# Optimization experiments

Measured on AMD Instinct MI355X. Metric: run time of the kernel, lower is better.

Reference implementation:

```python
import jax, jax.numpy as jnp
import numpy as np

SPACING = 0.25
CHANNELS = 32
MAX_VAL = 5.0
ENC_FEATS = 128
GRID_N = int(round(2 * MAX_VAL / SPACING)) + 1  # 41
BATCH = 131072

# Uniform cubic B-spline basis matrix: weights(t) = [1, t, t^2, t^3] @ M
CUBIC_B_SPLINE_MATRIX = (1.0 / 6.0) * jnp.array(
    [[1.0, 4.0, 1.0, 0.0],
     [-3.0, 0.0, 3.0, 0.0],
     [3.0, -6.0, 3.0, 0.0],
     [-1.0, 3.0, -3.0, 1.0]], dtype=jnp.float32)


def setup_inputs() -> dict:
    key = jax.random.key(0)
    k1, k2, k3, k4 = jax.random.split(key, 4)
    nb_params = jax.random.normal(k1, (BATCH, 3), dtype=jnp.float32) * 3.0
    lig_grid = jax.random.normal(k2, (CHANNELS, GRID_N, GRID_N, GRID_N), dtype=jnp.float32) * 0.1
    enc_w = jax.random.normal(k3, (ENC_FEATS, CHANNELS), dtype=jnp.float32) / np.sqrt(CHANNELS)
    enc_b = jax.random.normal(k4, (ENC_FEATS,), dtype=jnp.float32) * 0.01
    return {"nb_params": nb_params, "lig_grid": lig_grid, "enc_w": enc_w, "enc_b": enc_b}


def interpolate_grid_3d(grid, coords, interp_matrix):
    # grid: [C, N, N, N]; coords in [0,1]^3: [B, 3]
    N = grid.shape[1]
    u = coords * (N - 1)                       # continuous grid coords [B,3]
    base = jnp.floor(u).astype(jnp.int32)
    t = u - base                               # fractional part [B,3]
    offs = jnp.arange(-1, 3, dtype=jnp.int32)  # 4-point cubic stencil
    idx = jnp.clip(base[:, None, :] + offs[None, :, None], 0, N - 1)  # [B,4,3]
    # per-axis B-spline weights: [B,3,4]
    tp = jnp.stack([jnp.ones_like(t), t, t * t, t * t * t], axis=-1)
    w = jnp.einsum('bdk,kj->bdj', tp, interp_matrix)
    ix, iy, iz = idx[:, :, 0], idx[:, :, 1], idx[:, :, 2]
    # gather 4x4x4 neighborhood: [C,B,4,4,4]
    vals = grid[:, ix[:, :, None, None], iy[:, None, :, None], iz[:, None, None, :]]
    # tricubic weighted sum -> [B,C]
    return jnp.einsum('cbijk,bi,bj,bk->bc', vals, w[:, 0], w[:, 1], w[:, 2])


def reference(nb_params, lig_grid, enc_w, enc_b):
    nb_norm = 0.5 + 0.5 * (nb_params / MAX_VAL)
    nb_norm = jnp.clip(nb_norm, 0.0, 1.0)
    lig_x = interpolate_grid_3d(lig_grid, nb_norm, CUBIC_B_SPLINE_MATRIX)  # [B,C]
    return lig_x @ enc_w.T + enc_b  # [B, ENC_FEATS]
```

## Files before the change

### kernel.cpp

```cpp
#include <hip/hip_runtime.h>
#include <hip/hip_fp16.h>
#include <cstdint>

constexpr int GN   = 41;
constexpr int VOX  = GN * GN * GN;
constexpr int CH   = 32;
constexpr int EF   = 128;
constexpr int TILE = 64;
constexpr int XPAD = 36;

typedef _Float16 h2 __attribute__((ext_vector_type(2)));

__device__ __forceinline__ uint32_t pack_h2(float a, float b) {
    __half2 h = __floats2half2_rn(a, b);
    return __builtin_bit_cast(uint32_t, h);
}

__global__ __launch_bounds__(256) void prep_k(
    const float* __restrict__ src, const float* __restrict__ enc_w,
    __half* __restrict__ gT, uint32_t* __restrict__ ewP) {
    int idx = blockIdx.x * 256 + threadIdx.x;
    if (idx < VOX * 4) {
        int s  = idx >> 2;
        int ck = idx & 3;
        float v[8];
#pragma unroll
        for (int i = 0; i < 8; ++i) v[i] = src[(ck * 8 + i) * VOX + s];
        *reinterpret_cast<uint4*>(gT + (size_t)s * CH + ck * 8) =
            make_uint4(pack_h2(v[0], v[1]), pack_h2(v[2], v[3]),
                       pack_h2(v[4], v[5]), pack_h2(v[6], v[7]));
    }
    int pid = idx - VOX * 4;
    if (pid >= 0 && pid < 512) {
        int f  = pid >> 2;
        int qq = pid & 3;
        const float* wr = enc_w + f * CH + qq * 8;
        float4 a = *reinterpret_cast<const float4*>(wr);
        float4 b = *reinterpret_cast<const float4*>(wr + 4);
        *reinterpret_cast<uint4*>(ewP + (size_t)pid * 4) =
            make_uint4(pack_h2(a.x, a.y), pack_h2(a.z, a.w),
                       pack_h2(b.x, b.y), pack_h2(b.z, b.w));
    }
}

__device__ __forceinline__ void bspline_w(float t, float w[4]) {
    float t2 = t * t, t3 = t2 * t;
    const float k = 1.0f / 6.0f;
    w[0] = k * (1.0f - 3.0f * t + 3.0f * t2 - t3);
    w[1] = k * (4.0f - 6.0f * t2 + 3.0f * t3);
    w[2] = k * (1.0f + 3.0f * t + 3.0f * t2 - 3.0f * t3);
    w[3] = k * t3;
}

__global__ __launch_bounds__(256, 4) void lig_main(
    const float* __restrict__ nb, const __half* __restrict__ gT,
    const uint32_t* __restrict__ ewP, const float* __restrict__ enc_b,
    float* __restrict__ out, int batch) {

    __shared__ __align__(16) float xs[TILE * XPAD];

    const int tid  = threadIdx.x;
    const int lane = tid & 63;
    const int wv   = tid >> 6;
    const int eq   = lane >> 4;
    const int zsl  = (lane >> 2) & 3;
    const int ck   = (lane & 3) * 8;
    const int base_e = blockIdx.x * TILE;

#pragma unroll 1
    for (int qi = 0; qi < 4; ++qi) {
        const int eloc = wv * 16 + qi * 4 + eq;
        const int e    = base_e + eloc;

        float p0 = nb[3 * e], p1 = nb[3 * e + 1], p2 = nb[3 * e + 2];
        float ux = fminf(fmaxf(0.5f + 0.1f * p0, 0.0f), 1.0f) * 40.0f;
        float uy = fminf(fmaxf(0.5f + 0.1f * p1, 0.0f), 1.0f) * 40.0f;
        float uz = fminf(fmaxf(0.5f + 0.1f * p2, 0.0f), 1.0f) * 40.0f;
        int bx = (int)ux, by = (int)uy, bz = (int)uz;
        float wx[4], wy[4], wz[4];
        bspline_w(ux - (float)bx, wx);
        bspline_w(uy - (float)by, wy);
        bspline_w(uz - (float)bz, wz);

        const float wzl = wz[zsl];
#pragma unroll
        for (int o = 0; o < 4; ++o) wx[o] *= wzl;

        int X[4], Y[4];
#pragma unroll
        for (int o = 0; o < 4; ++o) {
            X[o] = min(max(bx + o - 1, 0), GN - 1) * (GN * GN * CH);
            Y[o] = min(max(by + o - 1, 0), GN - 1) * (GN * CH);
        }
        const int Zoff = min(max(bz + zsl - 1, 0), GN - 1) * CH + ck;

        float acc[8];
#pragma unroll
        for (int k = 0; k < 8; ++k) acc[k] = 0.0f;

#pragma unroll
        for (int i = 0; i < 4; ++i) {
#pragma unroll
            for (int j = 0; j < 4; ++j) {
                const uint4 raw =
                    *reinterpret_cast<const uint4*>(gT + (X[i] + Y[j] + Zoff));
                const float wt = wx[i] * wy[j];
                float2 f0 = __half22float2(__builtin_bit_cast(__half2, raw.x));
                float2 f1 = __half22float2(__builtin_bit_cast(__half2, raw.y));
                float2 f2 = __half22float2(__builtin_bit_cast(__half2, raw.z));
                float2 f3 = __half22float2(__builtin_bit_cast(__half2, raw.w));
                acc[0] = fmaf(wt, f0.x, acc[0]);
                acc[1] = fmaf(wt, f0.y, acc[1]);
                acc[2] = fmaf(wt, f1.x, acc[2]);
                acc[3] = fmaf(wt, f1.y, acc[3]);
                acc[4] = fmaf(wt, f2.x, acc[4]);
                acc[5] = fmaf(wt, f2.y, acc[5]);
                acc[6] = fmaf(wt, f3.x, acc[6]);
                acc[7] = fmaf(wt, f3.y, acc[7]);
            }
        }

#pragma unroll
        for (int k = 0; k < 8; ++k) {
            acc[k] += __shfl_xor(acc[k], 4);
            acc[k] += __shfl_xor(acc[k], 8);
        }

        if ((lane & 12) == 0) {
            float* dst = xs + eloc * XPAD + ck;
            *reinterpret_cast<float4*>(dst) =
                make_float4(acc[0], acc[1], acc[2], acc[3]);
            *reinterpret_cast<float4*>(dst + 4) =
                make_float4(acc[4], acc[5], acc[6], acc[7]);
        }
    }
    __syncthreads();

    const int e_loc = lane;
    const int fq    = __builtin_amdgcn_readfirstlane(wv);
    const int e     = base_e + e_loc;

    h2 xp[16];
#pragma unroll
    for (int g = 0; g < 8; ++g) {
        float4 v = *reinterpret_cast<const float4*>(&xs[e_loc * XPAD + g * 4]);
        xp[2 * g]     = __builtin_bit_cast(h2, __builtin_amdgcn_cvt_pkrtz(v.x, v.y));
        xp[2 * g + 1] = __builtin_bit_cast(h2, __builtin_amdgcn_cvt_pkrtz(v.z, v.w));
    }

    const uint32_t* wbase = ewP + (size_t)fq * 32 * 16;
    const float*    bbase = enc_b + fq * 32;
    float*          obase = out + (size_t)e * EF + fq * 32;

#pragma unroll 4
    for (int f = 0; f < 32; ++f) {
        const uint32_t* wr = wbase + f * 16;
        float s = bbase[f];
#pragma unroll
        for (int p = 0; p < 16; ++p)
            s = __builtin_amdgcn_fdot2(xp[p], __builtin_bit_cast(h2, wr[p]),
                                       s, false);
        obase[f] = s;
    }
}

extern "C" void kernel_launch(void* const* d_in, const int* in_sizes, int n_in,
                              void* d_out, int out_size, void* d_ws,
                              size_t ws_size, hipStream_t stream) {
    const float* nb   = (const float*)d_in[0];
    const float* grid = (const float*)d_in[1];
    const float* ew   = (const float*)d_in[2];
    const float* eb   = (const float*)d_in[3];
    float*       out  = (float*)d_out;
    __half*      gTh  = (__half*)d_ws;
    uint32_t*    ewP  = (uint32_t*)(gTh + (size_t)VOX * CH);

    int batch = in_sizes[0] / 3;

    int prep_blocks = (VOX * 4 + 512 + 255) / 256;
    prep_k<<<prep_blocks, 256, 0, stream>>>(grid, ew, gTh, ewP);
    lig_main<<<batch / TILE, 256, 0, stream>>>(nb, gTh, ewP, eb, out, batch);
}
```

Baseline: 131.1 us.

## Use fma_mix for half accumulation and remap encoder so lanes own output features

The gather loop now uses v_fma_mix_f32 inline asm to multiply fp16 grid values by fp32 weights directly, which removes the separate half-to-float conversions. Interpolated features are packed to fp16 in shared memory. The encoder stage is restructured so each lane keeps two weight rows in registers and loops over the wave's 16 elements, reading broadcast fp16 activations from LDS. Output stores become coalesced float2 rows instead of strided per-element writes. The __syncthreads is removed on the basis that each wave only reads the LDS rows it wrote itself.

```diff
diff --git a/kernel.cpp b/kernel.cpp
--- a/kernel.cpp
+++ b/kernel.cpp
@@ -7,7 +7,6 @@
 constexpr int CH   = 32;
 constexpr int EF   = 128;
 constexpr int TILE = 64;
-constexpr int XPAD = 36;
 
 typedef _Float16 h2 __attribute__((ext_vector_type(2)));
 
@@ -52,12 +51,21 @@
     w[3] = k * t3;
 }
 
+__device__ __forceinline__ void fma_mix_lo(float& a, float w, uint32_t p) {
+    asm("v_fma_mix_f32 %0, %1, %2, %0 op_sel:[0,0,0] op_sel_hi:[0,1,0]"
+        : "+v"(a) : "v"(w), "v"(p));
+}
+__device__ __forceinline__ void fma_mix_hi(float& a, float w, uint32_t p) {
+    asm("v_fma_mix_f32 %0, %1, %2, %0 op_sel:[0,1,0] op_sel_hi:[0,1,0]"
+        : "+v"(a) : "v"(w), "v"(p));
+}
+
 __global__ __launch_bounds__(256, 4) void lig_main(
     const float* __restrict__ nb, const __half* __restrict__ gT,
     const uint32_t* __restrict__ ewP, const float* __restrict__ enc_b,
     float* __restrict__ out, int batch) {
 
-    __shared__ __align__(16) float xs[TILE * XPAD];
+    __shared__ __align__(16) uint32_t xs[TILE * 16];
 
     const int tid  = threadIdx.x;
     const int lane = tid & 63;
@@ -66,6 +74,7 @@
     const int zsl  = (lane >> 2) & 3;
     const int ck   = (lane & 3) * 8;
     const int base_e = blockIdx.x * TILE;
+    (void)batch;
 
 #pragma unroll 1
     for (int qi = 0; qi < 4; ++qi) {
@@ -105,18 +114,14 @@
                 const uint4 raw =
                     *reinterpret_cast<const uint4*>(gT + (X[i] + Y[j] + Zoff));
                 const float wt = wx[i] * wy[j];
-                float2 f0 = __half22float2(__builtin_bit_cast(__half2, raw.x));
-                float2 f1 = __half22float2(__builtin_bit_cast(__half2, raw.y));
-                float2 f2 = __half22float2(__builtin_bit_cast(__half2, raw.z));
-                float2 f3 = __half22float2(__builtin_bit_cast(__half2, raw.w));
-                acc[0] = fmaf(wt, f0.x, acc[0]);
-                acc[1] = fmaf(wt, f0.y, acc[1]);
-                acc[2] = fmaf(wt, f1.x, acc[2]);
-                acc[3] = fmaf(wt, f1.y, acc[3]);
-                acc[4] = fmaf(wt, f2.x, acc[4]);
-                acc[5] = fmaf(wt, f2.y, acc[5]);
-                acc[6] = fmaf(wt, f3.x, acc[6]);
-                acc[7] = fmaf(wt, f3.y, acc[7]);
+                fma_mix_lo(acc[0], wt, raw.x);
+                fma_mix_hi(acc[1], wt, raw.x);
+                fma_mix_lo(acc[2], wt, raw.y);
+                fma_mix_hi(acc[3], wt, raw.y);
+                fma_mix_lo(acc[4], wt, raw.z);
+                fma_mix_hi(acc[5], wt, raw.z);
+                fma_mix_lo(acc[6], wt, raw.w);
+                fma_mix_hi(acc[7], wt, raw.w);
             }
         }
 
@@ -127,40 +132,58 @@
         }
 
         if ((lane & 12) == 0) {
-            float* dst = xs + eloc * XPAD + ck;
-            *reinterpret_cast<float4*>(dst) =
-                make_float4(acc[0], acc[1], acc[2], acc[3]);
-            *reinterpret_cast<float4*>(dst + 4) =
-                make_float4(acc[4], acc[5], acc[6], acc[7]);
-        }
-    }
-    __syncthreads();
-
-    const int e_loc = lane;
-    const int fq    = __builtin_amdgcn_readfirstlane(wv);
-    const int e     = base_e + e_loc;
-
-    h2 xp[16];
-#pragma unroll
-    for (int g = 0; g < 8; ++g) {
-        float4 v = *reinterpret_cast<const float4*>(&xs[e_loc * XPAD + g * 4]);
-        xp[2 * g]     = __builtin_bit_cast(h2, __builtin_amdgcn_cvt_pkrtz(v.x, v.y));
-        xp[2 * g + 1] = __builtin_bit_cast(h2, __builtin_amdgcn_cvt_pkrtz(v.z, v.w));
-    }
-
-    const uint32_t* wbase = ewP + (size_t)fq * 32 * 16;
-    const float*    bbase = enc_b + fq * 32;
-    float*          obase = out + (size_t)e * EF + fq * 32;
+            uint32_t d0 = __builtin_bit_cast(
+                uint32_t, __builtin_amdgcn_cvt_pkrtz(acc[0], acc[1]));
+            uint32_t d1 = __builtin_bit_cast(
+                uint32_t, __builtin_amdgcn_cvt_pkrtz(acc[2], acc[3]));
+            uint32_t d2 = __builtin_bit_cast(
+                uint32_t, __builtin_amdgcn_cvt_pkrtz(acc[4], acc[5]));
+            uint32_t d3 = __builtin_bit_cast(
+                uint32_t, __builtin_amdgcn_cvt_pkrtz(acc[6], acc[7]));
+            *reinterpret_cast<uint4*>(&xs[eloc * 16 + (lane & 3) * 4]) =
+                make_uint4(d0, d1, d2, d3);
+        }
+    }
+
+    const int f0 = lane * 2;
+    uint32_t w0[16], w1[16];
+    {
+        const uint4* wp0 = reinterpret_cast<const uint4*>(ewP + (size_t)f0 * 16);
+        const uint4* wp1 = reinterpret_cast<const uint4*>(ewP + (size_t)(f0 + 1) * 16);
+#pragma unroll
+        for (int g = 0; g < 4; ++g) {
+            uint4 a = wp0[g];
+            w0[4 * g + 0] = a.x; w0[4 * g + 1] = a.y;
+            w0[4 * g + 2] = a.z; w0[4 * g + 3] = a.w;
+            uint4 b = wp1[g];
+            w1[4 * g + 0] = b.x; w1[4 * g + 1] = b.y;
+            w1[4 * g + 2] = b.z; w1[4 * g + 3] = b.w;
+        }
+    }
+    const float2 bb = *reinterpret_cast<const float2*>(enc_b + f0);
+
+    float*          obase = out + (size_t)(base_e + wv * 16) * EF + f0;
+    const uint32_t* xbase = xs + (size_t)(wv * 16) * 16;
 
 #pragma unroll 4
-    for (int f = 0; f < 32; ++f) {
-        const uint32_t* wr = wbase + f * 16;
-        float s = bbase[f];
-#pragma unroll
-        for (int p = 0; p < 16; ++p)
-            s = __builtin_amdgcn_fdot2(xp[p], __builtin_bit_cast(h2, wr[p]),
-                                       s, false);
-        obase[f] = s;
+    for (int i = 0; i < 16; ++i) {
+        const uint32_t* xp = xbase + i * 16;
+        uint4 x0 = *reinterpret_cast<const uint4*>(xp);
+        uint4 x1 = *reinterpret_cast<const uint4*>(xp + 4);
+        uint4 x2 = *reinterpret_cast<const uint4*>(xp + 8);
+        uint4 x3 = *reinterpret_cast<const uint4*>(xp + 12);
+        uint32_t xd[16] = {x0.x, x0.y, x0.z, x0.w, x1.x, x1.y, x1.z, x1.w,
+                           x2.x, x2.y, x2.z, x2.w, x3.x, x3.y, x3.z, x3.w};
+        float s0 = bb.x, s1 = bb.y;
+#pragma unroll
+        for (int p = 0; p < 16; ++p) {
+            s0 = __builtin_amdgcn_fdot2(__builtin_bit_cast(h2, xd[p]),
+                                        __builtin_bit_cast(h2, w0[p]), s0, false);
+            s1 = __builtin_amdgcn_fdot2(__builtin_bit_cast(h2, xd[p]),
+                                        __builtin_bit_cast(h2, w1[p]), s1, false);
+        }
+        *reinterpret_cast<float2*>(obase + (size_t)i * EF) =
+            make_float2(s0, s1);
     }
 }
 
```

Result: faster. 123.9 us (-5.5%).
